# Kernel optimization log

Hardware: AMD Instinct MI355X
Metric: run time of the kernel (lower is better)

Reference implementation:

```python
import jax, jax.numpy as jnp
import numpy as np

N_NODES = 10000
N_EDGES = 160000
MUL0, MUL1 = 32, 8            # multiplicities of 0e and 1o irreps
IN_DIM = MUL0 + 3 * MUL1      # 56
EDGE_FEAT = 64
HIDDEN = 64
# FullyConnectedTensorProduct paths (in x sh -> out):
# (0e,0e)->0e : 32*32=1024 ; (0e,1o)->1o : 32*8=256
# (1o,0e)->1o : 8*8=64     ; (1o,1o)->0e : 8*32=256
W_NUMEL = 1024 + 256 + 64 + 256  # 1600
PATH_NORM = 1.0 / np.sqrt(MUL0 + MUL1)  # 'element' path normalization (fan_in=40)
CG_110 = 1.0 / np.sqrt(3.0)             # normalized w3j for 1x1->0


def setup_inputs() -> dict:
    key = jax.random.key(0)
    ks = jax.random.split(key, 8)
    node_attr = jax.random.normal(ks[0], (N_NODES, IN_DIM), jnp.float32)
    edge_index = jax.random.randint(ks[1], (2, N_EDGES), 0, N_NODES, jnp.int64 if jax.config.read('jax_enable_x64') else jnp.int32)
    edge_attr = jax.random.normal(ks[2], (N_EDGES, EDGE_FEAT), jnp.float32)
    edge_sh = jax.random.normal(ks[3], (N_EDGES, 4), jnp.float32)
    fc_w1 = jax.random.normal(ks[4], (EDGE_FEAT, HIDDEN), jnp.float32) / np.sqrt(EDGE_FEAT)
    fc_b1 = jnp.zeros((HIDDEN,), jnp.float32)
    fc_w2 = jax.random.normal(ks[5], (HIDDEN, W_NUMEL), jnp.float32) / np.sqrt(HIDDEN)
    fc_b2 = jnp.zeros((W_NUMEL,), jnp.float32)
    return {"node_attr": node_attr, "edge_attr": edge_attr, "edge_sh": edge_sh,
            "fc_w1": fc_w1, "fc_b1": fc_b1, "fc_w2": fc_w2, "fc_b2": fc_b2,
            "edge_index": edge_index}


def _tp(x, sh, w):
    # x: [E,56] gathered node feats, sh: [E,4], w: [E,1600] per-edge TP weights
    x0 = x[:, :MUL0]                       # [E,32]   0e scalars
    x1 = x[:, MUL0:].reshape(-1, MUL1, 3)  # [E,8,3]  1o vectors
    sh0 = sh[:, :1]                        # [E,1]
    sh1 = sh[:, 1:4]                       # [E,3]
    w1 = w[:, :1024].reshape(-1, MUL0, MUL0)        # (0e,0e)->0e
    w2 = w[:, 1024:1280].reshape(-1, MUL0, MUL1)    # (0e,1o)->1o
    w3 = w[:, 1280:1344].reshape(-1, MUL1, MUL1)    # (1o,0e)->1o
    w4 = w[:, 1344:1600].reshape(-1, MUL1, MUL0)    # (1o,1o)->0e
    out0 = (jnp.einsum('euv,eu->ev', w1, x0) * sh0
            + CG_110 * jnp.einsum('euv,eum,em->ev', w4, x1, sh1)) * PATH_NORM  # [E,32]
    out1 = (jnp.einsum('euv,eu,em->evm', w2, x0, sh1)
            + jnp.einsum('euv,eum->evm', w3, x1) * sh0[:, :, None]) * PATH_NORM  # [E,8,3]
    return jnp.concatenate([out0, out1.reshape(-1, 3 * MUL1)], axis=-1)  # [E,56]


def reference(node_attr, edge_attr, edge_sh, fc_w1, fc_b1, fc_w2, fc_b2, edge_index):
    edge_src, edge_dst = edge_index[0], edge_index[1]
    # edge MLP -> per-edge tensor-product weights
    h = jax.nn.relu(edge_attr @ fc_w1 + fc_b1)
    w = h @ fc_w2 + fc_b2                                  # [E,1600]
    tp = _tp(node_attr[edge_dst], edge_sh, w)              # gather + TP, [E,56]
    # scatter-mean to source nodes
    n = node_attr.shape[0]
    summed = jax.ops.segment_sum(tp, edge_src, num_segments=n)
    counts = jax.ops.segment_sum(jnp.ones(edge_src.shape, tp.dtype), edge_src, num_segments=n)
    out = summed / jnp.maximum(counts, 1.0)[:, None]
    # residual (pad node_attr up to out width; 0 here since in==out irreps)
    pad = out.shape[-1] - node_attr.shape[-1]
    out = out + jnp.pad(node_attr, ((0, 0), (0, pad)))
    return out
```

## Files before the change

### kernel.cpp

```cpp
#include <hip/hip_runtime.h>

#define NN 10000
#define NE 160000
#define IND 56
#define WN 1600
#define EPB 128
#define NBLK (NE / EPB)
#define DCAP 64

typedef __attribute__((ext_vector_type(8))) short bf16x8;
typedef __attribute__((ext_vector_type(4))) float f32x4;

static constexpr float PATH_NORM_C = 0.15811388300841897f;
static constexpr float CG_C        = 0.57735026918962576f;

__device__ __forceinline__ uint32_t f2bf(float f) {
    uint32_t x = __float_as_uint(f);
    return (x + 0x7fffu + ((x >> 16) & 1u)) >> 16;
}
__device__ __forceinline__ uint32_t pack2(float a, float b) {
    return f2bf(a) | (f2bf(b) << 16);
}
__device__ __forceinline__ f32x4 ld_cf4(const ushort* p) {
    uint2 w = *reinterpret_cast<const uint2*>(p);
// ... 13 lines not shown
{
    int i = blockIdx.x * 256 + threadIdx.x;
    if (i < 64 * 64) {
        int k = i >> 6, j = i & 63;
        W1T[k * 64 + j] = (ushort)f2bf(fc_w1[j * 64 + k]);
    }
    int i2 = i - 64 * 64;
    if (i2 >= 0 && i2 < 100 * 1024) {
        int t  = i2 >> 10, r = i2 & 1023;
        int kh = r >> 9,  rr = r & 511;
        int l  = rr >> 3, ii = rr & 7;
        int j  = t * 16 + (l & 15);
        int k  = kh * 32 + ((l >> 4) << 3) + ii;
        W2F[i2] = (ushort)f2bf(fc_w2[k * WN + j]);
    }
    int i3 = i2 - 100 * 1024;
    if (i3 >= 0 && i3 < NE && do_fill) {
        int s = edge_index[i3];
        int pos = atomicAdd(&cursor[s], 1);
        if (pos < DCAP) elist[s * DCAP + pos] = i3;
    }
}

__global__ __launch_bounds__(256, 3) void edge_kernel(
    const float* __restrict__ node_attr,
    const float* __restrict__ edge_attr,
    const float* __restrict__ edge_sh,
    const float* __restrict__ fc_b1,
    const float* __restrict__ fc_b2,
    const int*   __restrict__ edge_index,
    const ushort* __restrict__ W1T,
    const ushort* __restrict__ W2F,
    float* __restrict__ tpbuf)
{
    __shared__ ushort cfh[64][EPB];
    __shared__ float  shS[4][EPB];
    __shared__ __attribute__((aligned(16))) ushort pool[8192];

    const int tid  = threadIdx.x;
    const int wave = tid >> 6;
    const int lane = tid & 63;
    const int g    = lane >> 4;
    const int q    = lane & 15;
    const int E0   = blockIdx.x * EPB;

    if (tid < EPB) {
        const int e    = tid;
// ... 8 lines not shown
        }
        #pragma unroll
        for (int u = 0; u < 32; ++u) cfh[u][e] = (ushort)f2bf(xr[u]);
        #pragma unroll
        for (int u = 0; u < 8; ++u) {
            cfh[32 + 3*u + 0][e] = (ushort)f2bf(sh.x * xr[32 + 3*u + 0]);
            cfh[32 + 3*u + 1][e] = (ushort)f2bf(sh.x * xr[32 + 3*u + 1]);
            cfh[32 + 3*u + 2][e] = (ushort)f2bf(sh.x * xr[32 + 3*u + 2]);
            cfh[56 + u][e] = (ushort)f2bf(
                CG_C * (xr[32+3*u]*sh.y + xr[32+3*u+1]*sh.z + xr[32+3*u+2]*sh.w));
        }
        shS[0][e] = sh.x;
        shS[1][e] = sh.y;  shS[2][e] = sh.z;  shS[3][e] = sh.w;
    }

    f32x4 d1[2][4];
    #pragma unroll
    for (int mt = 0; mt < 4; ++mt) {
        const float4 b1v = *reinterpret_cast<const float4*>(fc_b1 + mt*16 + 4*g);
        #pragma unroll
        for (int ms = 0; ms < 2; ++ms)
            d1[ms][mt] = (f32x4){b1v.x, b1v.y, b1v.z, b1v.w};
    }

    #pragma unroll
    for (int kh = 0; kh < 2; ++kh) {
        bf16x8 bfr[2];
        #pragma unroll
        for (int ms = 0; ms < 2; ++ms) {
            const int e = E0 + wave*32 + ms*16 + q;
            const float* ap = edge_attr + (size_t)e * 64 + kh*32 + g*8;
            float4 f0 = *reinterpret_cast<const float4*>(ap);
            float4 f1 = *reinterpret_cast<const float4*>(ap + 4);
            union { uint32_t u[4]; bf16x8 v; } cv;
            cv.u[0] = pack2(f0.x, f0.y); cv.u[1] = pack2(f0.z, f0.w);
            cv.u[2] = pack2(f1.x, f1.y); cv.u[3] = pack2(f1.z, f1.w);
            bfr[ms] = cv.v;
        }
        #pragma unroll
        for (int mt = 0; mt < 4; ++mt) {
            bf16x8 afr = *reinterpret_cast<const bf16x8*>(W1T + (mt*16 + q)*64 + kh*32 + g*8);
            #pragma unroll
            for (int ms = 0; ms < 2; ++ms)
                d1[ms][mt] = __builtin_amdgcn_mfma_f32_16x16x32_bf16(afr, bfr[ms], d1[ms][mt], 0, 0, 0);
        }
    }
    #pragma unroll
// ... 239 lines not shown

__global__ __launch_bounds__(256) void gather_kernel(
    const float* __restrict__ tpbuf, const int* __restrict__ cursor,
    const int* __restrict__ elist, const float* __restrict__ node_attr,
    float* __restrict__ out)
{
    const int node = blockIdx.x * 4 + (threadIdx.x >> 6);
    const int j = threadIdx.x & 63;
    if (node >= NN) return;
    const int degt = cursor[node];
    const int deg = (degt < DCAP) ? degt : DCAP;
    float sum = 0.f;
    #pragma unroll 4
    for (int i = 0; i < deg; ++i) {
        const int e = elist[node * DCAP + i];
        if (j < 56) sum += tpbuf[(size_t)e * IND + j];
    }
    if (j < 56) {
        const float c = (degt > 0) ? (float)degt : 1.f;
        out[node * IND + j] = sum / c + node_attr[node * IND + j];
    }
}

__global__ __launch_bounds__(256, 3) void edge_kernel_fb(
    const float* __restrict__ node_attr, const float* __restrict__ edge_attr,
    const float* __restrict__ edge_sh, const float* __restrict__ fc_b1,
    const float* __restrict__ fc_b2, const int* __restrict__ edge_index,
    const ushort* __restrict__ W1T, const ushort* __restrict__ W2F,
    float* __restrict__ acc, float* __restrict__ cnt)
{
    __shared__ ushort cfh[64][EPB];
    __shared__ float  shS[4][EPB];
    __shared__ int    src_lds[EPB];
    __shared__ __attribute__((aligned(16))) ushort pool[8192];

    const int tid  = threadIdx.x;
    const int wave = tid >> 6;
    const int lane = tid & 63;
    const int g    = lane >> 4;
    const int q    = lane & 15;
    const int E0   = blockIdx.x * EPB;

    if (tid < EPB) {
        const int e    = tid;
        const int srcn = edge_index[E0 + e];
        const int dstn = edge_index[NE + E0 + e];
        src_lds[e] = srcn;
        const float4 sh = reinterpret_cast<const float4*>(edge_sh)[E0 + e];
        const float4* xp = reinterpret_cast<const float4*>(node_attr + (size_t)dstn * IND);
        float xr[56];
        #pragma unroll
        for (int i = 0; i < 14; ++i) {
            float4 v = xp[i];
            xr[4*i] = v.x; xr[4*i+1] = v.y; xr[4*i+2] = v.z; xr[4*i+3] = v.w;
        }
        #pragma unroll
        for (int u = 0; u < 32; ++u) cfh[u][e] = (ushort)f2bf(xr[u]);
        #pragma unroll
        for (int u = 0; u < 8; ++u) {
            cfh[32 + 3*u + 0][e] = (ushort)f2bf(sh.x * xr[32 + 3*u + 0]);
            cfh[32 + 3*u + 1][e] = (ushort)f2bf(sh.x * xr[32 + 3*u + 1]);
            cfh[32 + 3*u + 2][e] = (ushort)f2bf(sh.x * xr[32 + 3*u + 2]);
            cfh[56 + u][e] = (ushort)f2bf(
                CG_C * (xr[32+3*u]*sh.y + xr[32+3*u+1]*sh.z + xr[32+3*u+2]*sh.w));
        }
        shS[0][e] = sh.x;
        shS[1][e] = sh.y;  shS[2][e] = sh.z;  shS[3][e] = sh.w;
    }

    f32x4 d1[2][4];
    #pragma unroll
    for (int mt = 0; mt < 4; ++mt) {
        const float4 b1v = *reinterpret_cast<const float4*>(fc_b1 + mt*16 + 4*g);
        #pragma unroll
        for (int ms = 0; ms < 2; ++ms)
            d1[ms][mt] = (f32x4){b1v.x, b1v.y, b1v.z, b1v.w};
    }
    #pragma unroll
    for (int kh = 0; kh < 2; ++kh) {
        bf16x8 bfr[2];
        #pragma unroll
        for (int ms = 0; ms < 2; ++ms) {
            const int e = E0 + wave*32 + ms*16 + q;
            const float* ap = edge_attr + (size_t)e * 64 + kh*32 + g*8;
            float4 f0 = *reinterpret_cast<const float4*>(ap);
            float4 f1 = *reinterpret_cast<const float4*>(ap + 4);
            union { uint32_t u[4]; bf16x8 v; } cv;
            cv.u[0] = pack2(f0.x, f0.y); cv.u[1] = pack2(f0.z, f0.w);
            cv.u[2] = pack2(f1.x, f1.y); cv.u[3] = pack2(f1.z, f1.w);
            bfr[ms] = cv.v;
        }
        #pragma unroll
        for (int mt = 0; mt < 4; ++mt) {
            bf16x8 afr = *reinterpret_cast<const bf16x8*>(W1T + (mt*16 + q)*64 + kh*32 + g*8);
            #pragma unroll
            for (int ms = 0; ms < 2; ++ms)
                d1[ms][mt] = __builtin_amdgcn_mfma_f32_16x16x32_bf16(afr, bfr[ms], d1[ms][mt], 0, 0, 0);
        }
    }
    #pragma unroll
    for (int mt = 0; mt < 4; ++mt) {
        const int kg = 2*mt + (g >> 1);
        #pragma unroll
        for (int ms = 0; ms < 2; ++ms) {
            float v0 = fmaxf(d1[ms][mt][0], 0.f);
            float v1 = fmaxf(d1[ms][mt][1], 0.f);
            float v2 = fmaxf(d1[ms][mt][2], 0.f);
            float v3 = fmaxf(d1[ms][mt][3], 0.f);
            uint32_t* wp = reinterpret_cast<uint32_t*>(
                &pool[wave*2048 + ms*1024 + (kg*16 + q)*8 + 4*(g & 1)]);
            wp[0] = pack2(v0, v1);
            wp[1] = pack2(v2, v3);
        }
    }
    bf16x8 af[2][2];
    #pragma unroll
    for (int ms = 0; ms < 2; ++ms)
        #pragma unroll
        for (int kh = 0; kh < 2; ++kh)
            af[ms][kh] = *reinterpret_cast<const bf16x8*>(
                &pool[wave*2048 + ms*1024 + ((kh*4 + g)*16 + q)*8]);

    bf16x8 A0, A1, B0, B1, C0, C1, D0, D1;
    float  Ab, Bb, Cb, Db;
    auto load_slot = [&](int t, bf16x8& b0, bf16x8& b1, float& bb) {
        const ushort* p = W2F + (size_t)t * 1024 + lane * 8;
        b0 = *reinterpret_cast<const bf16x8*>(p);
        b1 = *reinterpret_cast<const bf16x8*>(p + 512);
        bb = fc_b2[t * 16 + q];
    };
    load_slot(0, A0, A1, Ab);
    load_slot(1, B0, B1, Bb);
    load_slot(2, C0, C1, Cb);
    load_slot(3, D0, D1, Db);
    __syncthreads();

    const int ebase = wave*32 + 4*g;
    f32x4 s0v[2];
    s0v[0] = *reinterpret_cast<const f32x4*>(&shS[0][ebase]);
    s0v[1] = *reinterpret_cast<const f32x4*>(&shS[0][ebase + 16]);
    float o0[2][2][4];
    float ttv[2][4];
    float o1v[2][4][3];
    #pragma unroll
    for (int ms = 0; ms < 2; ++ms)
        #pragma unroll
        for (int r = 0; r < 4; ++r) {
            o0[ms][0][r] = 0.f; o0[ms][1][r] = 0.f; ttv[ms][r] = 0.f;
            o1v[ms][r][0] = 0.f; o1v[ms][r][1] = 0.f; o1v[ms][r][2] = 0.f;
        }
    auto mfma2 = [&](const bf16x8& b0, const bf16x8& b1, float b2v, f32x4* accv) {
        #pragma unroll
        for (int ms = 0; ms < 2; ++ms) {
            f32x4 a = (f32x4){b2v, b2v, b2v, b2v};
            a = __builtin_amdgcn_mfma_f32_16x16x32_bf16(af[ms][0], b0, a, 0, 0, 0);
            a = __builtin_amdgcn_mfma_f32_16x16x32_bf16(af[ms][1], b1, a, 0, 0, 0);
            accv[ms] = a;
        }
    };
    const int qh = q >> 3;
    #pragma unroll 1
    for (int c = 0; c < 16; ++c) {
        const int t4 = 4*c;
        const int u0 = 2*c, u1 = 2*c + 1;
        f32x4 c00 = ld_cf4(&cfh[u0][ebase]);
        f32x4 c01 = ld_cf4(&cfh[u0][ebase + 16]);
        f32x4 c10 = ld_cf4(&cfh[u1][ebase]);
        f32x4 c11 = ld_cf4(&cfh[u1][ebase + 16]);
        f32x4 w2[2];
        mfma2(A0, A1, Ab, w2);  load_slot(t4 + 4, A0, A1, Ab);
        #pragma unroll
        for (int r = 0; r < 4; ++r) {
            o0[0][0][r] = fmaf(s0v[0][r]*c00[r], w2[0][r], o0[0][0][r]);
            o0[1][0][r] = fmaf(s0v[1][r]*c01[r], w2[1][r], o0[1][0][r]);
        }
        mfma2(B0, B1, Bb, w2);  load_slot(t4 + 5, B0, B1, Bb);
        #pragma unroll
        for (int r = 0; r < 4; ++r) {
            o0[0][1][r] = fmaf(s0v[0][r]*c00[r], w2[0][r], o0[0][1][r]);
            o0[1][1][r] = fmaf(s0v[1][r]*c01[r], w2[1][r], o0[1][1][r]);
        }
        mfma2(C0, C1, Cb, w2);  load_slot(t4 + 6, C0, C1, Cb);
        #pragma unroll
        for (int r = 0; r < 4; ++r) {
            o0[0][0][r] = fmaf(s0v[0][r]*c10[r], w2[0][r], o0[0][0][r]);
            o0[1][0][r] = fmaf(s0v[1][r]*c11[r], w2[1][r], o0[1][0][r]);
        }
        mfma2(D0, D1, Db, w2);  load_slot(t4 + 7, D0, D1, Db);
        #pragma unroll
        for (int r = 0; r < 4; ++r) {
            o0[0][1][r] = fmaf(s0v[0][r]*c10[r], w2[0][r], o0[0][1][r]);
            o0[1][1][r] = fmaf(s0v[1][r]*c11[r], w2[1][r], o0[1][1][r]);
        }
    }
    #pragma unroll 1
    for (int d = 0; d < 4; ++d) {
        const int t4 = 64 + 4*d;
        f32x4 w2[2];
        mfma2(A0, A1, Ab, w2);  load_slot(t4 + 4, A0, A1, Ab);
        {
            const int u = 8*d + qh;
            #pragma unroll
            for (int ms = 0; ms < 2; ++ms) {
                f32x4 cfv = ld_cf4(&cfh[u][ebase + ms*16]);
                #pragma unroll
                for (int r = 0; r < 4; ++r) ttv[ms][r] = fmaf(cfv[r], w2[ms][r], ttv[ms][r]);
            }
        }
        mfma2(B0, B1, Bb, w2);  load_slot(t4 + 5, B0, B1, Bb);
        {
            const int u = 8*d + 2 + qh;
            #pragma unroll
            for (int ms = 0; ms < 2; ++ms) {
                f32x4 cfv = ld_cf4(&cfh[u][ebase + ms*16]);
                #pragma unroll
                for (int r = 0; r < 4; ++r) ttv[ms][r] = fmaf(cfv[r], w2[ms][r], ttv[ms][r]);
            }
        }
        mfma2(C0, C1, Cb, w2);  load_slot(t4 + 6, C0, C1, Cb);
        {
            const int u = 8*d + 4 + qh;
            #pragma unroll
            for (int ms = 0; ms < 2; ++ms) {
                f32x4 cfv = ld_cf4(&cfh[u][ebase + ms*16]);
                #pragma unroll
                for (int r = 0; r < 4; ++r) ttv[ms][r] = fmaf(cfv[r], w2[ms][r], ttv[ms][r]);
            }
        }
        mfma2(D0, D1, Db, w2);  load_slot(t4 + 7, D0, D1, Db);
        {
            const int u = 8*d + 6 + qh;
            #pragma unroll
            for (int ms = 0; ms < 2; ++ms) {
                f32x4 cfv = ld_cf4(&cfh[u][ebase + ms*16]);
                #pragma unroll
                for (int r = 0; r < 4; ++r) ttv[ms][r] = fmaf(cfv[r], w2[ms][r], ttv[ms][r]);
            }
        }
    }
    {
        f32x4 w2[2];
        #define R3_BODY(TC)                                                         \
            {                                                                       \
                const int u = 2*(TC) + qh;                                          \
                _Pragma("unroll")                                                   \
                for (int ms = 0; ms < 2; ++ms)                                      \
                    _Pragma("unroll")                                               \
                    for (int m = 0; m < 3; ++m) {                                   \
                        f32x4 cfv = ld_cf4(&cfh[32 + u*3 + m][ebase + ms*16]);      \
                        _Pragma("unroll")                                           \
                        for (int r = 0; r < 4; ++r)                                 \
                            o1v[ms][r][m] = fmaf(cfv[r], w2[ms][r], o1v[ms][r][m]); \
                    }                                                               \
            }
        mfma2(A0, A1, Ab, w2);  load_slot(84, A0, A1, Ab);  R3_BODY(0)
        mfma2(B0, B1, Bb, w2);  load_slot(85, B0, B1, Bb);  R3_BODY(1)
        mfma2(C0, C1, Cb, w2);  load_slot(86, C0, C1, Cb);  R3_BODY(2)
        mfma2(D0, D1, Db, w2);  load_slot(87, D0, D1, Db);  R3_BODY(3)
        #undef R3_BODY
    }
    #pragma unroll 1
    for (int d = 0; d < 4; ++d) {
        const int t4 = 84 + 4*d;
        const int u0 = 2*d, u1 = 2*d + 1;
        f32x4 c00 = ld_cf4(&cfh[56 + u0][ebase]);
        f32x4 c01 = ld_cf4(&cfh[56 + u0][ebase + 16]);
        f32x4 c10 = ld_cf4(&cfh[56 + u1][ebase]);
        f32x4 c11 = ld_cf4(&cfh[56 + u1][ebase + 16]);
        f32x4 w2[2];
        int tn;
        mfma2(A0, A1, Ab, w2);  tn = t4 + 4; load_slot(tn < 100 ? tn : 99, A0, A1, Ab);
        #pragma unroll
        for (int r = 0; r < 4; ++r) {
            o0[0][0][r] = fmaf(c00[r], w2[0][r], o0[0][0][r]);
            o0[1][0][r] = fmaf(c01[r], w2[1][r], o0[1][0][r]);
        }
        mfma2(B0, B1, Bb, w2);  tn = t4 + 5; load_slot(tn < 100 ? tn : 99, B0, B1, Bb);
        #pragma unroll
        for (int r = 0; r < 4; ++r) {
            o0[0][1][r] = fmaf(c00[r], w2[0][r], o0[0][1][r]);
            o0[1][1][r] = fmaf(c01[r], w2[1][r], o0[1][1][r]);
        }
        mfma2(C0, C1, Cb, w2);  tn = t4 + 6; load_slot(tn < 100 ? tn : 99, C0, C1, Cb);
        #pragma unroll
        for (int r = 0; r < 4; ++r) {
            o0[0][0][r] = fmaf(c10[r], w2[0][r], o0[0][0][r]);
            o0[1][0][r] = fmaf(c11[r], w2[1][r], o0[1][0][r]);
        }
        mfma2(D0, D1, Db, w2);  tn = t4 + 7; load_slot(tn < 100 ? tn : 99, D0, D1, Db);
        #pragma unroll
        for (int r = 0; r < 4; ++r) {
            o0[0][1][r] = fmaf(c10[r], w2[0][r], o0[0][1][r]);
            o0[1][1][r] = fmaf(c11[r], w2[1][r], o0[1][1][r]);
        }
    }
    #pragma unroll
    for (int ms = 0; ms < 2; ++ms)
        #pragma unroll
        for (int r = 0; r < 4; ++r) {
            ttv[ms][r] += __shfl_xor(ttv[ms][r], 8, 64);
            #pragma unroll
            for (int m = 0; m < 3; ++m)
                o1v[ms][r][m] += __shfl_xor(o1v[ms][r][m], 8, 64);
        }
    #pragma unroll
    for (int ms = 0; ms < 2; ++ms) {
        const int eb = ebase + ms*16;
        const int4 srcv = *reinterpret_cast<const int4*>(&src_lds[eb]);
        const f32x4 s1x = *reinterpret_cast<const f32x4*>(&shS[1][eb]);
        const f32x4 s1y = *reinterpret_cast<const f32x4*>(&shS[2][eb]);
        const f32x4 s1z = *reinterpret_cast<const f32x4*>(&shS[3][eb]);
        #pragma unroll
        for (int r = 0; r < 4; ++r) {
            const int node = (r == 0) ? srcv.x : (r == 1) ? srcv.y : (r == 2) ? srcv.z : srcv.w;
            float* ap = acc + (size_t)node * IND;
            atomicAdd(ap + q,      PATH_NORM_C * o0[ms][0][r]);
            atomicAdd(ap + 16 + q, PATH_NORM_C * o0[ms][1][r]);
            if ((q & 8) == 0) {
                const int v = q & 7;
                atomicAdd(ap + 32 + 3*v + 0, PATH_NORM_C * (o1v[ms][r][0] + s1x[r]*ttv[ms][r]));
                atomicAdd(ap + 32 + 3*v + 1, PATH_NORM_C * (o1v[ms][r][1] + s1y[r]*ttv[ms][r]));
                atomicAdd(ap + 32 + 3*v + 2, PATH_NORM_C * (o1v[ms][r][2] + s1z[r]*ttv[ms][r]));
            }
        }
    }
    if (lane < 32) atomicAdd(cnt + src_lds[wave*32 + lane], 1.0f);
}

__global__ __launch_bounds__(256) void finalize_kernel(
    const float* __restrict__ acc, const float* __restrict__ cnt,
    const float* __restrict__ node_attr, float* __restrict__ out)
{
    const int i = blockIdx.x * 256 + threadIdx.x;
    if (i >= NN * IND) return;
    const int n = i / IND;
    const float c = fmaxf(cnt[n], 1.0f);
    out[i] = acc[i] / c + node_attr[i];
}

extern "C" void kernel_launch(void* const* d_in, const int* in_sizes, int n_in,
                              void* d_out, int out_size, void* d_ws, size_t ws_size,
                              hipStream_t stream) {
    const float* node_attr = (const float*)d_in[0];
    const float* edge_attr = (const float*)d_in[1];
    const float* edge_sh   = (const float*)d_in[2];
    const float* fc_w1     = (const float*)d_in[3];
    const float* fc_b1     = (const float*)d_in[4];
    const float* fc_w2     = (const float*)d_in[5];
    const float* fc_b2     = (const float*)d_in[6];
    const int*   edge_index = (const int*)d_in[7];

    char* ws = (char*)d_ws;
    int*    cursor = (int*)(ws + 0);
    int*    elist  = (int*)(ws + 40000);
    ushort* W1T    = (ushort*)(ws + 2600000);
    ushort* W2F    = (ushort*)(ws + 2608192);
    float*  tpbuf  = (float*)(ws + 2812992);
    const size_t WS_NEEDED = 2812992ull + (size_t)NE * IND * 4;

    if (ws_size >= WS_NEEDED) {
        hipMemsetAsync(cursor, 0, 40000, stream);
        prep_kernel<<<(64*64 + 100*1024 + NE + 255) / 256, 256, 0, stream>>>(
            fc_w1, fc_w2, edge_index, W1T, W2F, cursor, elist, 1);
        edge_kernel<<<NBLK, 256, 0, stream>>>(
            node_attr, edge_attr, edge_sh, fc_b1, fc_b2, edge_index, W1T, W2F, tpbuf);
        gather_kernel<<<(NN + 3) / 4, 256, 0, stream>>>(
            tpbuf, cursor, elist, node_attr, (float*)d_out);
    } else {
        float*  acc  = (float*)ws;
        float*  cnt  = (float*)(ws + 2240000);
        ushort* W1Tf = (ushort*)(ws + 2280000);
        ushort* W2Ff = (ushort*)(ws + 2288192);
        hipMemsetAsync(ws, 0, 2280000, stream);
        prep_kernel<<<(64*64 + 100*1024 + NE + 255) / 256, 256, 0, stream>>>(
            fc_w1, fc_w2, edge_index, W1Tf, W2Ff, (int*)W1Tf, (int*)W1Tf, 0);
        edge_kernel_fb<<<NBLK, 256, 0, stream>>>(
            node_attr, edge_attr, edge_sh, fc_b1, fc_b2, edge_index, W1Tf, W2Ff, acc, cnt);
        finalize_kernel<<<(NN * IND + 255) / 256, 256, 0, stream>>>(
            acc, cnt, node_attr, (float*)d_out);
    }
}
```

Measured before the change: 111.6 us.

## Split edge MLP first layer into separate kernel writing bf16 hidden buffer

Moves the first MLP layer (edge_attr @ W1 + relu) into its own h_kernel, which writes packed bf16 hidden activations in MFMA fragment layout to a workspace buffer. The main edge kernel then loads those fragments directly, which frees its LDS pool and drops the min-blocks launch bound, aiming for lower register and LDS pressure and better occupancy. The cost is an extra kernel launch and a global round trip of the hidden activations. The fallback path is replaced by a simple scalar per-edge kernel, and the split path only runs when the workspace is large enough.

```diff
diff --git a/kernel.cpp b/kernel.cpp
--- a/kernel.cpp
+++ b/kernel.cpp
@@ -59,7 +59,338 @@
     }
 }
 
-__global__ __launch_bounds__(256, 3) void edge_kernel(
+__global__ __launch_bounds__(256) void h_kernel(
+    const float* __restrict__ edge_attr,
+    const float* __restrict__ fc_b1,
+    const ushort* __restrict__ W1T,
+    ushort* __restrict__ Hbuf)
+{
+    const int tid  = threadIdx.x;
+    const int wave = tid >> 6;
+    const int lane = tid & 63;
+    const int g    = lane >> 4;
+    const int q    = lane & 15;
+    const int E0   = blockIdx.x * EPB;
+
+    f32x4 d1[2][4];
+    #pragma unroll
+    for (int mt = 0; mt < 4; ++mt) {
+        const float4 b1v = *reinterpret_cast<const float4*>(fc_b1 + mt*16 + 4*g);
+        #pragma unroll
+        for (int ms = 0; ms < 2; ++ms)
+            d1[ms][mt] = (f32x4){b1v.x, b1v.y, b1v.z, b1v.w};
+    }
+
+    #pragma unroll
+    for (int kh = 0; kh < 2; ++kh) {
+        bf16x8 bfr[2];
+        #pragma unroll
+        for (int ms = 0; ms < 2; ++ms) {
+            const int e = E0 + wave*32 + ms*16 + q;
+            const float* ap = edge_attr + (size_t)e * 64 + kh*32 + g*8;
+            float4 f0 = *reinterpret_cast<const float4*>(ap);
+            float4 f1 = *reinterpret_cast<const float4*>(ap + 4);
+            union { uint32_t u[4]; bf16x8 v; } cv;
+            cv.u[0] = pack2(f0.x, f0.y); cv.u[1] = pack2(f0.z, f0.w);
+            cv.u[2] = pack2(f1.x, f1.y); cv.u[3] = pack2(f1.z, f1.w);
+            bfr[ms] = cv.v;
+        }
+        #pragma unroll
+        for (int mt = 0; mt < 4; ++mt) {
+            bf16x8 afr = *reinterpret_cast<const bf16x8*>(W1T + (mt*16 + q)*64 + kh*32 + g*8);
+            #pragma unroll
+            for (int ms = 0; ms < 2; ++ms)
+                d1[ms][mt] = __builtin_amdgcn_mfma_f32_16x16x32_bf16(afr, bfr[ms], d1[ms][mt], 0, 0, 0);
+        }
+    }
+    #pragma unroll
+    for (int mt = 0; mt < 4; ++mt) {
+        const int kg = 2*mt + (g >> 1);
+        #pragma unroll
+        for (int ms = 0; ms < 2; ++ms) {
+            const int group = blockIdx.x*8 + wave*2 + ms;
+            float v0 = fmaxf(d1[ms][mt][0], 0.f);
+            float v1 = fmaxf(d1[ms][mt][1], 0.f);
+            float v2 = fmaxf(d1[ms][mt][2], 0.f);
+            float v3 = fmaxf(d1[ms][mt][3], 0.f);
+            uint2 w;
+            w.x = pack2(v0, v1);
+            w.y = pack2(v2, v3);
+            *reinterpret_cast<uint2*>(Hbuf + (size_t)group*1024 + (kg*16 + q)*8 + 4*(g & 1)) = w;
+        }
+    }
+}
+
+__global__ __launch_bounds__(256) void edge_kernel_split(
+    const float* __restrict__ node_attr,
+    const float* __restrict__ edge_sh,
+    const float* __restrict__ fc_b2,
+    const int*   __restrict__ edge_index,
+    const ushort* __restrict__ W2F,
+    const ushort* __restrict__ Hbuf,
+    float* __restrict__ tpbuf)
+{
+    __shared__ ushort cfh[64][EPB];
+    __shared__ float  shS[4][EPB];
+
+    const int tid  = threadIdx.x;
+    const int wave = tid >> 6;
+    const int lane = tid & 63;
+    const int g    = lane >> 4;
+    const int q    = lane & 15;
+    const int E0   = blockIdx.x * EPB;
+
+    if (tid < EPB) {
+        const int e    = tid;
+        const int dstn = edge_index[NE + E0 + e];
+        const float4 sh = reinterpret_cast<const float4*>(edge_sh)[E0 + e];
+        const float4* xp = reinterpret_cast<const float4*>(node_attr + (size_t)dstn * IND);
+        float xr[56];
+        #pragma unroll
+        for (int i = 0; i < 14; ++i) {
+            float4 v = xp[i];
+            xr[4*i] = v.x; xr[4*i+1] = v.y; xr[4*i+2] = v.z; xr[4*i+3] = v.w;
+        }
+        #pragma unroll
+        for (int u = 0; u < 32; ++u) cfh[u][e] = (ushort)f2bf(xr[u]);
+        #pragma unroll
+        for (int u = 0; u < 8; ++u) {
+            cfh[32 + 3*u + 0][e] = (ushort)f2bf(sh.x * xr[32 + 3*u + 0]);
+            cfh[32 + 3*u + 1][e] = (ushort)f2bf(sh.x * xr[32 + 3*u + 1]);
+            cfh[32 + 3*u + 2][e] = (ushort)f2bf(sh.x * xr[32 + 3*u + 2]);
+            cfh[56 + u][e] = (ushort)f2bf(
+                CG_C * (xr[32+3*u]*sh.y + xr[32+3*u+1]*sh.z + xr[32+3*u+2]*sh.w));
+        }
+        shS[0][e] = sh.x;
+        shS[1][e] = sh.y;  shS[2][e] = sh.z;  shS[3][e] = sh.w;
+    }
+
+    bf16x8 af[2][2];
+    #pragma unroll
+    for (int ms = 0; ms < 2; ++ms)
+        #pragma unroll
+        for (int kh = 0; kh < 2; ++kh)
+            af[ms][kh] = *reinterpret_cast<const bf16x8*>(
+                Hbuf + (size_t)(blockIdx.x*8 + wave*2 + ms)*1024 + kh*512 + g*128 + q*8);
+
+    bf16x8 A0, A1, B0, B1, C0, C1, D0, D1;
+    float  Ab, Bb, Cb, Db;
+    auto load_slot = [&](int t, bf16x8& b0, bf16x8& b1, float& bb) {
+        const ushort* p = W2F + (size_t)t * 1024 + lane * 8;
+        b0 = *reinterpret_cast<const bf16x8*>(p);
+        b1 = *reinterpret_cast<const bf16x8*>(p + 512);
+        bb = fc_b2[t * 16 + q];
+    };
+    load_slot(0, A0, A1, Ab);
+    load_slot(1, B0, B1, Bb);
+    load_slot(2, C0, C1, Cb);
+    load_slot(3, D0, D1, Db);
+
+    __syncthreads();
+
+    const int ebase = wave*32 + 4*g;
+    f32x4 s0v[2];
+    s0v[0] = *reinterpret_cast<const f32x4*>(&shS[0][ebase]);
+    s0v[1] = *reinterpret_cast<const f32x4*>(&shS[0][ebase + 16]);
+
+    float o0[2][2][4];
+    float ttv[2][4];
+    float o1v[2][4][3];
+    #pragma unroll
+    for (int ms = 0; ms < 2; ++ms) {
+        #pragma unroll
+        for (int r = 0; r < 4; ++r) {
+            o0[ms][0][r] = 0.f; o0[ms][1][r] = 0.f; ttv[ms][r] = 0.f;
+            o1v[ms][r][0] = 0.f; o1v[ms][r][1] = 0.f; o1v[ms][r][2] = 0.f;
+        }
+    }
+
+    auto mfma2 = [&](const bf16x8& b0, const bf16x8& b1, float b2v, f32x4* accv) {
+        #pragma unroll
+        for (int ms = 0; ms < 2; ++ms) {
+            f32x4 a = (f32x4){b2v, b2v, b2v, b2v};
+            a = __builtin_amdgcn_mfma_f32_16x16x32_bf16(af[ms][0], b0, a, 0, 0, 0);
+            a = __builtin_amdgcn_mfma_f32_16x16x32_bf16(af[ms][1], b1, a, 0, 0, 0);
+            accv[ms] = a;
+        }
+    };
+
+    const int qh = q >> 3;
+
+    #pragma unroll 1
+    for (int c = 0; c < 16; ++c) {
+        const int t4 = 4*c;
+        const int u0 = 2*c, u1 = 2*c + 1;
+        f32x4 c00 = ld_cf4(&cfh[u0][ebase]);
+        f32x4 c01 = ld_cf4(&cfh[u0][ebase + 16]);
+        f32x4 c10 = ld_cf4(&cfh[u1][ebase]);
+        f32x4 c11 = ld_cf4(&cfh[u1][ebase + 16]);
+        f32x4 w2[2];
+
+        mfma2(A0, A1, Ab, w2);  load_slot(t4 + 4, A0, A1, Ab);
+        #pragma unroll
+        for (int r = 0; r < 4; ++r) {
+            o0[0][0][r] = fmaf(s0v[0][r]*c00[r], w2[0][r], o0[0][0][r]);
+            o0[1][0][r] = fmaf(s0v[1][r]*c01[r], w2[1][r], o0[1][0][r]);
+        }
+        mfma2(B0, B1, Bb, w2);  load_slot(t4 + 5, B0, B1, Bb);
+        #pragma unroll
+        for (int r = 0; r < 4; ++r) {
+            o0[0][1][r] = fmaf(s0v[0][r]*c00[r], w2[0][r], o0[0][1][r]);
+            o0[1][1][r] = fmaf(s0v[1][r]*c01[r], w2[1][r], o0[1][1][r]);
+        }
+        mfma2(C0, C1, Cb, w2);  load_slot(t4 + 6, C0, C1, Cb);
+        #pragma unroll
+        for (int r = 0; r < 4; ++r) {
+            o0[0][0][r] = fmaf(s0v[0][r]*c10[r], w2[0][r], o0[0][0][r]);
+            o0[1][0][r] = fmaf(s0v[1][r]*c11[r], w2[1][r], o0[1][0][r]);
+        }
+        mfma2(D0, D1, Db, w2);  load_slot(t4 + 7, D0, D1, Db);
+        #pragma unroll
+        for (int r = 0; r < 4; ++r) {
+            o0[0][1][r] = fmaf(s0v[0][r]*c10[r], w2[0][r], o0[0][1][r]);
+            o0[1][1][r] = fmaf(s0v[1][r]*c11[r], w2[1][r], o0[1][1][r]);
+        }
+    }
+
+    #pragma unroll 1
+    for (int d = 0; d < 4; ++d) {
+        const int t4 = 64 + 4*d;
+        f32x4 w2[2];
+
+        mfma2(A0, A1, Ab, w2);  load_slot(t4 + 4, A0, A1, Ab);
+        {
+            const int u = 8*d + qh;
+            #pragma unroll
+            for (int ms = 0; ms < 2; ++ms) {
+                f32x4 cfv = ld_cf4(&cfh[u][ebase + ms*16]);
+                #pragma unroll
+                for (int r = 0; r < 4; ++r) ttv[ms][r] = fmaf(cfv[r], w2[ms][r], ttv[ms][r]);
+            }
+        }
+        mfma2(B0, B1, Bb, w2);  load_slot(t4 + 5, B0, B1, Bb);
+        {
+            const int u = 8*d + 2 + qh;
+            #pragma unroll
+            for (int ms = 0; ms < 2; ++ms) {
+                f32x4 cfv = ld_cf4(&cfh[u][ebase + ms*16]);
+                #pragma unroll
+                for (int r = 0; r < 4; ++r) ttv[ms][r] = fmaf(cfv[r], w2[ms][r], ttv[ms][r]);
+            }
+        }
+        mfma2(C0, C1, Cb, w2);  load_slot(t4 + 6, C0, C1, Cb);
+        {
+            const int u = 8*d + 4 + qh;
+            #pragma unroll
+            for (int ms = 0; ms < 2; ++ms) {
+                f32x4 cfv = ld_cf4(&cfh[u][ebase + ms*16]);
+                #pragma unroll
+                for (int r = 0; r < 4; ++r) ttv[ms][r] = fmaf(cfv[r], w2[ms][r], ttv[ms][r]);
+            }
+        }
+        mfma2(D0, D1, Db, w2);  load_slot(t4 + 7, D0, D1, Db);
+        {
+            const int u = 8*d + 6 + qh;
+            #pragma unroll
+            for (int ms = 0; ms < 2; ++ms) {
+                f32x4 cfv = ld_cf4(&cfh[u][ebase + ms*16]);
+                #pragma unroll
+                for (int r = 0; r < 4; ++r) ttv[ms][r] = fmaf(cfv[r], w2[ms][r], ttv[ms][r]);
+            }
+        }
+    }
+
+    {
+        f32x4 w2[2];
+        #define R3_BODY(TC)                                                         \
+            {                                                                       \
+                const int u = 2*(TC) + qh;                                          \
+                _Pragma("unroll")                                                   \
+                for (int ms = 0; ms < 2; ++ms)                                      \
+                    _Pragma("unroll")                                               \
+                    for (int m = 0; m < 3; ++m) {                                   \
+                        f32x4 cfv = ld_cf4(&cfh[32 + u*3 + m][ebase + ms*16]);      \
+                        _Pragma("unroll")                                           \
+                        for (int r = 0; r < 4; ++r)                                 \
+                            o1v[ms][r][m] = fmaf(cfv[r], w2[ms][r], o1v[ms][r][m]); \
+                    }                                                               \
+            }
+        mfma2(A0, A1, Ab, w2);  load_slot(84, A0, A1, Ab);  R3_BODY(0)
+        mfma2(B0, B1, Bb, w2);  load_slot(85, B0, B1, Bb);  R3_BODY(1)
+        mfma2(C0, C1, Cb, w2);  load_slot(86, C0, C1, Cb);  R3_BODY(2)
+        mfma2(D0, D1, Db, w2);  load_slot(87, D0, D1, Db);  R3_BODY(3)
+        #undef R3_BODY
+    }
+
+    #pragma unroll 1
+    for (int d = 0; d < 4; ++d) {
+        const int t4 = 84 + 4*d;
+        const int u0 = 2*d, u1 = 2*d + 1;
+        f32x4 c00 = ld_cf4(&cfh[56 + u0][ebase]);
+        f32x4 c01 = ld_cf4(&cfh[56 + u0][ebase + 16]);
+        f32x4 c10 = ld_cf4(&cfh[56 + u1][ebase]);
+        f32x4 c11 = ld_cf4(&cfh[56 + u1][ebase + 16]);
+        f32x4 w2[2];
+        int tn;
+
+        mfma2(A0, A1, Ab, w2);  tn = t4 + 4; load_slot(tn < 100 ? tn : 99, A0, A1, Ab);
+        #pragma unroll
+        for (int r = 0; r < 4; ++r) {
+            o0[0][0][r] = fmaf(c00[r], w2[0][r], o0[0][0][r]);
+            o0[1][0][r] = fmaf(c01[r], w2[1][r], o0[1][0][r]);
+        }
+        mfma2(B0, B1, Bb, w2);  tn = t4 + 5; load_slot(tn < 100 ? tn : 99, B0, B1, Bb);
+        #pragma unroll
+        for (int r = 0; r < 4; ++r) {
+            o0[0][1][r] = fmaf(c00[r], w2[0][r], o0[0][1][r]);
+            o0[1][1][r] = fmaf(c01[r], w2[1][r], o0[1][1][r]);
+        }
+        mfma2(C0, C1, Cb, w2);  tn = t4 + 6; load_slot(tn < 100 ? tn : 99, C0, C1, Cb);
+        #pragma unroll
+        for (int r = 0; r < 4; ++r) {
+            o0[0][0][r] = fmaf(c10[r], w2[0][r], o0[0][0][r]);
+            o0[1][0][r] = fmaf(c11[r], w2[1][r], o0[1][0][r]);
+        }
+        mfma2(D0, D1, Db, w2);  tn = t4 + 7; load_slot(tn < 100 ? tn : 99, D0, D1, Db);
+        #pragma unroll
+        for (int r = 0; r < 4; ++r) {
+            o0[0][1][r] = fmaf(c10[r], w2[0][r], o0[0][1][r]);
+            o0[1][1][r] = fmaf(c11[r], w2[1][r], o0[1][1][r]);
+        }
+    }
+
+    #pragma unroll
+    for (int ms = 0; ms < 2; ++ms)
+        #pragma unroll
+        for (int r = 0; r < 4; ++r) {
+            ttv[ms][r] += __shfl_xor(ttv[ms][r], 8, 64);
+            #pragma unroll
+            for (int m = 0; m < 3; ++m)
+                o1v[ms][r][m] += __shfl_xor(o1v[ms][r][m], 8, 64);
+        }
+
+    #pragma unroll
+    for (int ms = 0; ms < 2; ++ms) {
+        const int eb = ebase + ms*16;
+        const f32x4 s1x = *reinterpret_cast<const f32x4*>(&shS[1][eb]);
+        const f32x4 s1y = *reinterpret_cast<const f32x4*>(&shS[2][eb]);
+        const f32x4 s1z = *reinterpret_cast<const f32x4*>(&shS[3][eb]);
+        #pragma unroll
+        for (int r = 0; r < 4; ++r) {
+            float* tp = tpbuf + (size_t)(E0 + eb + r) * IND;
+            tp[q]      = PATH_NORM_C * o0[ms][0][r];
+            tp[16 + q] = PATH_NORM_C * o0[ms][1][r];
+            if ((q & 8) == 0) {
+                const int v = q & 7;
+                tp[32 + 3*v + 0] = PATH_NORM_C * (o1v[ms][r][0] + s1x[r]*ttv[ms][r]);
+                tp[32 + 3*v + 1] = PATH_NORM_C * (o1v[ms][r][1] + s1y[r]*ttv[ms][r]);
+                tp[32 + 3*v + 2] = PATH_NORM_C * (o1v[ms][r][2] + s1z[r]*ttv[ms][r]);
+            }
+        }
+    }
+}
+
+__global__ __launch_bounds__(256, 3) void edge_kernel_mono(
     const float* __restrict__ node_attr,
     const float* __restrict__ edge_attr,
     const float* __restrict__ edge_sh,
@@ -114,7 +445,6 @@
         for (int ms = 0; ms < 2; ++ms)
             d1[ms][mt] = (f32x4){b1v.x, b1v.y, b1v.z, b1v.w};
     }
-
     #pragma unroll
     for (int kh = 0; kh < 2; ++kh) {
         bf16x8 bfr[2];
@@ -400,312 +730,7 @@
     }
 }
 
-__global__ __launch_bounds__(256, 3) void edge_kernel_fb(
-    const float* __restrict__ node_attr, const float* __restrict__ edge_attr,
-    const float* __restrict__ edge_sh, const float* __restrict__ fc_b1,
-    const float* __restrict__ fc_b2, const int* __restrict__ edge_index,
-    const ushort* __restrict__ W1T, const ushort* __restrict__ W2F,
-    float* __restrict__ acc, float* __restrict__ cnt)
-{
-    __shared__ ushort cfh[64][EPB];
-    __shared__ float  shS[4][EPB];
-    __shared__ int    src_lds[EPB];
-    __shared__ __attribute__((aligned(16))) ushort pool[8192];
-
-    const int tid  = threadIdx.x;
-    const int wave = tid >> 6;
-    const int lane = tid & 63;
-    const int g    = lane >> 4;
-    const int q    = lane & 15;
-    const int E0   = blockIdx.x * EPB;
-
-    if (tid < EPB) {
-        const int e    = tid;
-        const int srcn = edge_index[E0 + e];
-        const int dstn = edge_index[NE + E0 + e];
-        src_lds[e] = srcn;
-        const float4 sh = reinterpret_cast<const float4*>(edge_sh)[E0 + e];
-        const float4* xp = reinterpret_cast<const float4*>(node_attr + (size_t)dstn * IND);
-        float xr[56];
-        #pragma unroll
-        for (int i = 0; i < 14; ++i) {
-            float4 v = xp[i];
-            xr[4*i] = v.x; xr[4*i+1] = v.y; xr[4*i+2] = v.z; xr[4*i+3] = v.w;
-        }
-        #pragma unroll
-        for (int u = 0; u < 32; ++u) cfh[u][e] = (ushort)f2bf(xr[u]);
-        #pragma unroll
-        for (int u = 0; u < 8; ++u) {
-            cfh[32 + 3*u + 0][e] = (ushort)f2bf(sh.x * xr[32 + 3*u + 0]);
-            cfh[32 + 3*u + 1][e] = (ushort)f2bf(sh.x * xr[32 + 3*u + 1]);
-            cfh[32 + 3*u + 2][e] = (ushort)f2bf(sh.x * xr[32 + 3*u + 2]);
-            cfh[56 + u][e] = (ushort)f2bf(
-                CG_C * (xr[32+3*u]*sh.y + xr[32+3*u+1]*sh.z + xr[32+3*u+2]*sh.w));
-        }
-        shS[0][e] = sh.x;
-        shS[1][e] = sh.y;  shS[2][e] = sh.z;  shS[3][e] = sh.w;
-    }
-
-    f32x4 d1[2][4];
-    #pragma unroll
-    for (int mt = 0; mt < 4; ++mt) {
-        const float4 b1v = *reinterpret_cast<const float4*>(fc_b1 + mt*16 + 4*g);
-        #pragma unroll
-        for (int ms = 0; ms < 2; ++ms)
-            d1[ms][mt] = (f32x4){b1v.x, b1v.y, b1v.z, b1v.w};
-    }
-    #pragma unroll
-    for (int kh = 0; kh < 2; ++kh) {
-        bf16x8 bfr[2];
-        #pragma unroll
-        for (int ms = 0; ms < 2; ++ms) {
-            const int e = E0 + wave*32 + ms*16 + q;
-            const float* ap = edge_attr + (size_t)e * 64 + kh*32 + g*8;
-            float4 f0 = *reinterpret_cast<const float4*>(ap);
-            float4 f1 = *reinterpret_cast<const float4*>(ap + 4);
-            union { uint32_t u[4]; bf16x8 v; } cv;
-            cv.u[0] = pack2(f0.x, f0.y); cv.u[1] = pack2(f0.z, f0.w);
-            cv.u[2] = pack2(f1.x, f1.y); cv.u[3] = pack2(f1.z, f1.w);
-            bfr[ms] = cv.v;
-        }
-        #pragma unroll
-        for (int mt = 0; mt < 4; ++mt) {
-            bf16x8 afr = *reinterpret_cast<const bf16x8*>(W1T + (mt*16 + q)*64 + kh*32 + g*8);
-            #pragma unroll
-            for (int ms = 0; ms < 2; ++ms)
-                d1[ms][mt] = __builtin_amdgcn_mfma_f32_16x16x32_bf16(afr, bfr[ms], d1[ms][mt], 0, 0, 0);
-        }
-    }
-    #pragma unroll
-    for (int mt = 0; mt < 4; ++mt) {
-        const int kg = 2*mt + (g >> 1);
-        #pragma unroll
-        for (int ms = 0; ms < 2; ++ms) {
-            float v0 = fmaxf(d1[ms][mt][0], 0.f);
-            float v1 = fmaxf(d1[ms][mt][1], 0.f);
-            float v2 = fmaxf(d1[ms][mt][2], 0.f);
-            float v3 = fmaxf(d1[ms][mt][3], 0.f);
-            uint32_t* wp = reinterpret_cast<uint32_t*>(
-                &pool[wave*2048 + ms*1024 + (kg*16 + q)*8 + 4*(g & 1)]);
-            wp[0] = pack2(v0, v1);
-            wp[1] = pack2(v2, v3);
-        }
-    }
-    bf16x8 af[2][2];
-    #pragma unroll
-    for (int ms = 0; ms < 2; ++ms)
-        #pragma unroll
-        for (int kh = 0; kh < 2; ++kh)
-            af[ms][kh] = *reinterpret_cast<const bf16x8*>(
-                &pool[wave*2048 + ms*1024 + ((kh*4 + g)*16 + q)*8]);
-
-    bf16x8 A0, A1, B0, B1, C0, C1, D0, D1;
-    float  Ab, Bb, Cb, Db;
-    auto load_slot = [&](int t, bf16x8& b0, bf16x8& b1, float& bb) {
-        const ushort* p = W2F + (size_t)t * 1024 + lane * 8;
-        b0 = *reinterpret_cast<const bf16x8*>(p);
-        b1 = *reinterpret_cast<const bf16x8*>(p + 512);
-        bb = fc_b2[t * 16 + q];
-    };
-    load_slot(0, A0, A1, Ab);
-    load_slot(1, B0, B1, Bb);
-    load_slot(2, C0, C1, Cb);
-    load_slot(3, D0, D1, Db);
-    __syncthreads();
-
-    const int ebase = wave*32 + 4*g;
-    f32x4 s0v[2];
-    s0v[0] = *reinterpret_cast<const f32x4*>(&shS[0][ebase]);
-    s0v[1] = *reinterpret_cast<const f32x4*>(&shS[0][ebase + 16]);
-    float o0[2][2][4];
-    float ttv[2][4];
-    float o1v[2][4][3];
-    #pragma unroll
-    for (int ms = 0; ms < 2; ++ms)
-        #pragma unroll
-        for (int r = 0; r < 4; ++r) {
-            o0[ms][0][r] = 0.f; o0[ms][1][r] = 0.f; ttv[ms][r] = 0.f;
-            o1v[ms][r][0] = 0.f; o1v[ms][r][1] = 0.f; o1v[ms][r][2] = 0.f;
-        }
-    auto mfma2 = [&](const bf16x8& b0, const bf16x8& b1, float b2v, f32x4* accv) {
-        #pragma unroll
-        for (int ms = 0; ms < 2; ++ms) {
-            f32x4 a = (f32x4){b2v, b2v, b2v, b2v};
-            a = __builtin_amdgcn_mfma_f32_16x16x32_bf16(af[ms][0], b0, a, 0, 0, 0);
-            a = __builtin_amdgcn_mfma_f32_16x16x32_bf16(af[ms][1], b1, a, 0, 0, 0);
-            accv[ms] = a;
-        }
-    };
-    const int qh = q >> 3;
-    #pragma unroll 1
-    for (int c = 0; c < 16; ++c) {
-        const int t4 = 4*c;
-        const int u0 = 2*c, u1 = 2*c + 1;
-        f32x4 c00 = ld_cf4(&cfh[u0][ebase]);
-        f32x4 c01 = ld_cf4(&cfh[u0][ebase + 16]);
-        f32x4 c10 = ld_cf4(&cfh[u1][ebase]);
-        f32x4 c11 = ld_cf4(&cfh[u1][ebase + 16]);
-        f32x4 w2[2];
-        mfma2(A0, A1, Ab, w2);  load_slot(t4 + 4, A0, A1, Ab);
-        #pragma unroll
-        for (int r = 0; r < 4; ++r) {
-            o0[0][0][r] = fmaf(s0v[0][r]*c00[r], w2[0][r], o0[0][0][r]);
-            o0[1][0][r] = fmaf(s0v[1][r]*c01[r], w2[1][r], o0[1][0][r]);
-        }
-        mfma2(B0, B1, Bb, w2);  load_slot(t4 + 5, B0, B1, Bb);
-        #pragma unroll
-        for (int r = 0; r < 4; ++r) {
-            o0[0][1][r] = fmaf(s0v[0][r]*c00[r], w2[0][r], o0[0][1][r]);
-            o0[1][1][r] = fmaf(s0v[1][r]*c01[r], w2[1][r], o0[1][1][r]);
-        }
-        mfma2(C0, C1, Cb, w2);  load_slot(t4 + 6, C0, C1, Cb);
-        #pragma unroll
-        for (int r = 0; r < 4; ++r) {
-            o0[0][0][r] = fmaf(s0v[0][r]*c10[r], w2[0][r], o0[0][0][r]);
-            o0[1][0][r] = fmaf(s0v[1][r]*c11[r], w2[1][r], o0[1][0][r]);
-        }
-        mfma2(D0, D1, Db, w2);  load_slot(t4 + 7, D0, D1, Db);
-        #pragma unroll
-        for (int r = 0; r < 4; ++r) {
-            o0[0][1][r] = fmaf(s0v[0][r]*c10[r], w2[0][r], o0[0][1][r]);
-            o0[1][1][r] = fmaf(s0v[1][r]*c11[r], w2[1][r], o0[1][1][r]);
-        }
-    }
-    #pragma unroll 1
-    for (int d = 0; d < 4; ++d) {
-        const int t4 = 64 + 4*d;
-        f32x4 w2[2];
-        mfma2(A0, A1, Ab, w2);  load_slot(t4 + 4, A0, A1, Ab);
-        {
-            const int u = 8*d + qh;
-            #pragma unroll
-            for (int ms = 0; ms < 2; ++ms) {
-                f32x4 cfv = ld_cf4(&cfh[u][ebase + ms*16]);
-                #pragma unroll
-                for (int r = 0; r < 4; ++r) ttv[ms][r] = fmaf(cfv[r], w2[ms][r], ttv[ms][r]);
-            }
-        }
-        mfma2(B0, B1, Bb, w2);  load_slot(t4 + 5, B0, B1, Bb);
-        {
-            const int u = 8*d + 2 + qh;
-            #pragma unroll
-            for (int ms = 0; ms < 2; ++ms) {
-                f32x4 cfv = ld_cf4(&cfh[u][ebase + ms*16]);
-                #pragma unroll
-                for (int r = 0; r < 4; ++r) ttv[ms][r] = fmaf(cfv[r], w2[ms][r], ttv[ms][r]);
-            }
-        }
-        mfma2(C0, C1, Cb, w2);  load_slot(t4 + 6, C0, C1, Cb);
-        {
-            const int u = 8*d + 4 + qh;
-            #pragma unroll
-            for (int ms = 0; ms < 2; ++ms) {
-                f32x4 cfv = ld_cf4(&cfh[u][ebase + ms*16]);
-                #pragma unroll
-                for (int r = 0; r < 4; ++r) ttv[ms][r] = fmaf(cfv[r], w2[ms][r], ttv[ms][r]);
-            }
-        }
-        mfma2(D0, D1, Db, w2);  load_slot(t4 + 7, D0, D1, Db);
-        {
-            const int u = 8*d + 6 + qh;
-            #pragma unroll
-            for (int ms = 0; ms < 2; ++ms) {
-                f32x4 cfv = ld_cf4(&cfh[u][ebase + ms*16]);
-                #pragma unroll
-                for (int r = 0; r < 4; ++r) ttv[ms][r] = fmaf(cfv[r], w2[ms][r], ttv[ms][r]);
-            }
-        }
-    }
-    {
-        f32x4 w2[2];
-        #define R3_BODY(TC)                                                         \
-            {                                                                       \
-                const int u = 2*(TC) + qh;                                          \
-                _Pragma("unroll")                                                   \
-                for (int ms = 0; ms < 2; ++ms)                                      \
-                    _Pragma("unroll")                                               \
-                    for (int m = 0; m < 3; ++m) {                                   \
-                        f32x4 cfv = ld_cf4(&cfh[32 + u*3 + m][ebase + ms*16]);      \
-                        _Pragma("unroll")                                           \
-                        for (int r = 0; r < 4; ++r)                                 \
-                            o1v[ms][r][m] = fmaf(cfv[r], w2[ms][r], o1v[ms][r][m]); \
-                    }                                                               \
-            }
-        mfma2(A0, A1, Ab, w2);  load_slot(84, A0, A1, Ab);  R3_BODY(0)
-        mfma2(B0, B1, Bb, w2);  load_slot(85, B0, B1, Bb);  R3_BODY(1)
-        mfma2(C0, C1, Cb, w2);  load_slot(86, C0, C1, Cb);  R3_BODY(2)
-        mfma2(D0, D1, Db, w2);  load_slot(87, D0, D1, Db);  R3_BODY(3)
-        #undef R3_BODY
-    }
-    #pragma unroll 1
-    for (int d = 0; d < 4; ++d) {
-        const int t4 = 84 + 4*d;
-        const int u0 = 2*d, u1 = 2*d + 1;
-        f32x4 c00 = ld_cf4(&cfh[56 + u0][ebase]);
-        f32x4 c01 = ld_cf4(&cfh[56 + u0][ebase + 16]);
-        f32x4 c10 = ld_cf4(&cfh[56 + u1][ebase]);
-        f32x4 c11 = ld_cf4(&cfh[56 + u1][ebase + 16]);
-        f32x4 w2[2];
-        int tn;
-        mfma2(A0, A1, Ab, w2);  tn = t4 + 4; load_slot(tn < 100 ? tn : 99, A0, A1, Ab);
-        #pragma unroll
-        for (int r = 0; r < 4; ++r) {
-            o0[0][0][r] = fmaf(c00[r], w2[0][r], o0[0][0][r]);
-            o0[1][0][r] = fmaf(c01[r], w2[1][r], o0[1][0][r]);
-        }
-        mfma2(B0, B1, Bb, w2);  tn = t4 + 5; load_slot(tn < 100 ? tn : 99, B0, B1, Bb);
-        #pragma unroll
-        for (int r = 0; r < 4; ++r) {
-            o0[0][1][r] = fmaf(c00[r], w2[0][r], o0[0][1][r]);
-            o0[1][1][r] = fmaf(c01[r], w2[1][r], o0[1][1][r]);
-        }
-        mfma2(C0, C1, Cb, w2);  tn = t4 + 6; load_slot(tn < 100 ? tn : 99, C0, C1, Cb);
-        #pragma unroll
-        for (int r = 0; r < 4; ++r) {
-            o0[0][0][r] = fmaf(c10[r], w2[0][r], o0[0][0][r]);
-            o0[1][0][r] = fmaf(c11[r], w2[1][r], o0[1][0][r]);
-        }
-        mfma2(D0, D1, Db, w2);  tn = t4 + 7; load_slot(tn < 100 ? tn : 99, D0, D1, Db);
-        #pragma unroll
-        for (int r = 0; r < 4; ++r) {
-            o0[0][1][r] = fmaf(c10[r], w2[0][r], o0[0][1][r]);
-            o0[1][1][r] = fmaf(c11[r], w2[1][r], o0[1][1][r]);
-        }
-    }
-    #pragma unroll
-    for (int ms = 0; ms < 2; ++ms)
-        #pragma unroll
-        for (int r = 0; r < 4; ++r) {
-            ttv[ms][r] += __shfl_xor(ttv[ms][r], 8, 64);
-            #pragma unroll
-            for (int m = 0; m < 3; ++m)
-                o1v[ms][r][m] += __shfl_xor(o1v[ms][r][m], 8, 64);
-        }
-    #pragma unroll
-    for (int ms = 0; ms < 2; ++ms) {
-        const int eb = ebase + ms*16;
-        const int4 srcv = *reinterpret_cast<const int4*>(&src_lds[eb]);
-        const f32x4 s1x = *reinterpret_cast<const f32x4*>(&shS[1][eb]);
-        const f32x4 s1y = *reinterpret_cast<const f32x4*>(&shS[2][eb]);
-        const f32x4 s1z = *reinterpret_cast<const f32x4*>(&shS[3][eb]);
-        #pragma unroll
-        for (int r = 0; r < 4; ++r) {
-            const int node = (r == 0) ? srcv.x : (r == 1) ? srcv.y : (r == 2) ? srcv.z : srcv.w;
-            float* ap = acc + (size_t)node * IND;
-            atomicAdd(ap + q,      PATH_NORM_C * o0[ms][0][r]);
-            atomicAdd(ap + 16 + q, PATH_NORM_C * o0[ms][1][r]);
-            if ((q & 8) == 0) {
-                const int v = q & 7;
-                atomicAdd(ap + 32 + 3*v + 0, PATH_NORM_C * (o1v[ms][r][0] + s1x[r]*ttv[ms][r]));
-                atomicAdd(ap + 32 + 3*v + 1, PATH_NORM_C * (o1v[ms][r][1] + s1y[r]*ttv[ms][r]));
-                atomicAdd(ap + 32 + 3*v + 2, PATH_NORM_C * (o1v[ms][r][2] + s1z[r]*ttv[ms][r]));
-            }
-        }
-    }
-    if (lane < 32) atomicAdd(cnt + src_lds[wave*32 + lane], 1.0f);
-}
-
-__global__ __launch_bounds__(256) void finalize_kernel(
+__global__ __launch_bounds__(256) void finalize_fb_kernel(
     const float* __restrict__ acc, const float* __restrict__ cnt,
     const float* __restrict__ node_attr, float* __restrict__ out)
 {
@@ -714,6 +739,75 @@
     const int n = i / IND;
     const float c = fmaxf(cnt[n], 1.0f);
     out[i] = acc[i] / c + node_attr[i];
+}
+
+__global__ __launch_bounds__(256) void edge_fb_kernel(
+    const float* __restrict__ node_attr, const float* __restrict__ edge_attr,
+    const float* __restrict__ edge_sh, const float* __restrict__ fc_w1,
+    const float* __restrict__ fc_b1, const float* __restrict__ fc_w2,
+    const float* __restrict__ fc_b2, const int* __restrict__ edge_index,
+    float* __restrict__ acc, float* __restrict__ cnt)
+{
+    const int idx = blockIdx.x * 256 + threadIdx.x;
+    if (idx >= NE) return;
+    const int e = idx;
+    const int src = edge_index[e];
+    const int dst = edge_index[NE + e];
+    float h[64];
+    #pragma unroll 1
+    for (int k = 0; k < 64; ++k) {
+        float s = fc_b1[k];
+        for (int j = 0; j < 64; ++j) s += edge_attr[(size_t)e*64 + j] * fc_w1[j*64 + k];
+        h[k] = fmaxf(s, 0.f);
+    }
+    const float4 sh = reinterpret_cast<const float4*>(edge_sh)[e];
+    const float* x = node_attr + (size_t)dst * IND;
+    float out0[32];
+    #pragma unroll 1
+    for (int v = 0; v < 32; ++v) out0[v] = 0.f;
+    float tt[8], o1[24];
+    #pragma unroll 1
+    for (int v = 0; v < 8; ++v) tt[v] = 0.f;
+    #pragma unroll 1
+    for (int i = 0; i < 24; ++i) o1[i] = 0.f;
+    #pragma unroll 1
+    for (int u = 0; u < 32; ++u) {
+        const float c1 = sh.x * x[u];
+        for (int v = 0; v < 32; ++v) {
+            float w = fc_b2[u*32 + v];
+            for (int k = 0; k < 64; ++k) w += h[k] * fc_w2[k*WN + u*32 + v];
+            out0[v] += c1 * w;
+        }
+        for (int v = 0; v < 8; ++v) {
+            float w = fc_b2[1024 + u*8 + v];
+            for (int k = 0; k < 64; ++k) w += h[k] * fc_w2[k*WN + 1024 + u*8 + v];
+            tt[v] += x[u] * w;
+        }
+    }
+    #pragma unroll 1
+    for (int u = 0; u < 8; ++u) {
+        const float y1 = CG_C * (x[32+3*u]*sh.y + x[32+3*u+1]*sh.z + x[32+3*u+2]*sh.w);
+        for (int v = 0; v < 8; ++v) {
+            float w = fc_b2[1280 + u*8 + v];
+            for (int k = 0; k < 64; ++k) w += h[k] * fc_w2[k*WN + 1280 + u*8 + v];
+            o1[3*v+0] += sh.x * w * x[32+3*u+0];
+            o1[3*v+1] += sh.x * w * x[32+3*u+1];
+            o1[3*v+2] += sh.x * w * x[32+3*u+2];
+        }
+        for (int v = 0; v < 32; ++v) {
+            float w = fc_b2[1344 + u*32 + v];
+            for (int k = 0; k < 64; ++k) w += h[k] * fc_w2[k*WN + 1344 + u*32 + v];
+            out0[v] += y1 * w;
+        }
+    }
+    float* ap = acc + (size_t)src * IND;
+    for (int v = 0; v < 32; ++v) atomicAdd(ap + v, PATH_NORM_C * out0[v]);
+    for (int v = 0; v < 8; ++v) {
+        atomicAdd(ap + 32 + 3*v + 0, PATH_NORM_C * (o1[3*v+0] + sh.y * tt[v]));
+        atomicAdd(ap + 32 + 3*v + 1, PATH_NORM_C * (o1[3*v+1] + sh.z * tt[v]));
+        atomicAdd(ap + 32 + 3*v + 2, PATH_NORM_C * (o1[3*v+2] + sh.w * tt[v]));
+    }
+    atomicAdd(cnt + src, 1.0f);
 }
 
 extern "C" void kernel_launch(void* const* d_in, const int* in_sizes, int n_in,
@@ -734,27 +828,31 @@
     ushort* W1T    = (ushort*)(ws + 2600000);
     ushort* W2F    = (ushort*)(ws + 2608192);
     float*  tpbuf  = (float*)(ws + 2812992);
-    const size_t WS_NEEDED = 2812992ull + (size_t)NE * IND * 4;
-
-    if (ws_size >= WS_NEEDED) {
+    ushort* Hbuf   = (ushort*)(ws + 38652992);
+    const size_t WS_SPLIT = 59132992ull;
+    const size_t WS_MONO  = 38652992ull;
+
+    if (ws_size >= WS_MONO) {
         hipMemsetAsync(cursor, 0, 40000, stream);
         prep_kernel<<<(64*64 + 100*1024 + NE + 255) / 256, 256, 0, stream>>>(
             fc_w1, fc_w2, edge_index, W1T, W2F, cursor, elist, 1);
-        edge_kernel<<<NBLK, 256, 0, stream>>>(
-            node_attr, edge_attr, edge_sh, fc_b1, fc_b2, edge_index, W1T, W2F, tpbuf);
+        if (ws_size >= WS_SPLIT) {
+            h_kernel<<<NBLK, 256, 0, stream>>>(edge_attr, fc_b1, W1T, Hbuf);
+            edge_kernel_split<<<NBLK, 256, 0, stream>>>(
+                node_attr, edge_sh, fc_b2, edge_index, W2F, Hbuf, tpbuf);
+        } else {
+            edge_kernel_mono<<<NBLK, 256, 0, stream>>>(
+                node_attr, edge_attr, edge_sh, fc_b1, fc_b2, edge_index, W1T, W2F, tpbuf);
+        }
         gather_kernel<<<(NN + 3) / 4, 256, 0, stream>>>(
             tpbuf, cursor, elist, node_attr, (float*)d_out);
     } else {
-        float*  acc  = (float*)ws;
-        float*  cnt  = (float*)(ws + 2240000);
-        ushort* W1Tf = (ushort*)(ws + 2280000);
-        ushort* W2Ff = (ushort*)(ws + 2288192);
+        float* acc = (float*)ws;
+        float* cnt = (float*)(ws + 2240000);
         hipMemsetAsync(ws, 0, 2280000, stream);
-        prep_kernel<<<(64*64 + 100*1024 + NE + 255) / 256, 256, 0, stream>>>(
-            fc_w1, fc_w2, edge_index, W1Tf, W2Ff, (int*)W1Tf, (int*)W1Tf, 0);
-        edge_kernel_fb<<<NBLK, 256, 0, stream>>>(
-            node_attr, edge_attr, edge_sh, fc_b1, fc_b2, edge_index, W1Tf, W2Ff, acc, cnt);
-        finalize_kernel<<<(NN * IND + 255) / 256, 256, 0, stream>>>(
+        edge_fb_kernel<<<(NE + 255) / 256, 256, 0, stream>>>(
+            node_attr, edge_attr, edge_sh, fc_w1, fc_b1, fc_w2, fc_b2, edge_index, acc, cnt);
+        finalize_fb_kernel<<<(NN * IND + 255) / 256, 256, 0, stream>>>(
             acc, cnt, node_attr, (float*)d_out);
     }
 }
```

Measured after the change: 113.9 us. +2.1%, slower.
